# Performance work log

Measured on AMD Instinct MI355X. Metric: run time of the kernel, lower is better.

## Reference

```python
import jax, jax.numpy as jnp
import numpy as np

INF = 1.0e10
EPS = 1e-12

def setup_inputs() -> dict:
    key = jax.random.key(0)
    k1, k2 = jax.random.split(key)
    B, N, A = 512, 16384, 64
    return {
        "residue_ca_pos": jax.random.normal(k1, (B, N, 3), dtype=jnp.float32) * 10.0,
        "residue_mask": jnp.ones((B, N), dtype=jnp.float32),
        "atom_pos": jax.random.normal(k2, (B, A, 3), dtype=jnp.float32) * 10.0,
        "atom_mask": jnp.ones((B, A), dtype=jnp.float32),
        "max_p": 1,
        "top_k": 4096,
    }

def reference(residue_ca_pos, residue_mask, atom_pos, atom_mask, max_p, top_k):
    # ligand centroid per batch: [B, 3]
    centroid = atom_pos.sum(-2) / atom_mask.sum(-1, keepdims=True)
    # distance from centroid to each residue Ca, invalid residues pushed to +inf
    diff = centroid[:, None, :] - residue_ca_pos            # [B, N, 3]
    dists = jnp.sqrt(jnp.sum(diff * diff, axis=-1) + EPS) + (1.0 - residue_mask) * INF
    # k smallest distances -> neighbor indices [B, top_k]
    _, nbr_indices = jax.lax.top_k(-dists, top_k)
    rows = jnp.arange(residue_mask.shape[0])[:, None]       # [B, 1]
    # scatter writes building the masks (faithful to torch scatter_ with constants)
    residue_spatial_mask = residue_mask.at[rows, nbr_indices].set(0.0)
    residue_spatial_mask_esm = (1.0 - residue_mask).at[rows, nbr_indices].set(32.0)
    return residue_spatial_mask, residue_spatial_mask_esm
```

## Files before the change

### kernel.cpp

```cpp
#include <hip/hip_runtime.h>

#pragma clang fp contract(off)

#define B_  512
#define N_  16384
#define A_  64
#define SL  8
#define EPT 8
#define CAP 2048

__global__ __launch_bounds__(256) void k1_dist(
    const float* __restrict__ pos,  const float* __restrict__ mask,
    const float* __restrict__ apos, const float* __restrict__ amask,
    float* __restrict__ centws, unsigned* __restrict__ hist_g,
    unsigned short* __restrict__ ws16)
{
#pragma clang fp contract(off)
    __shared__ unsigned hist[2048];
    __shared__ float s_c[3];
    const int tid = threadIdx.x;
    const int blk = blockIdx.x;
    const int b = blk >> 3, sl = blk & 7;

#pragma unroll
    for (int i = 0; i < 8; ++i) hist[tid + i * 256] = 0u;

    if (tid < 64) {
        const float* ap = apos  + (size_t)b * (A_ * 3);
        const float* am = amask + (size_t)b * A_;
        float comp = 0.0f, ms = 0.0f;
        if (tid < 3) {
            comp = ap[tid];
            for (int a = 1; a < A_; ++a) comp += ap[a * 3 + tid];
        }
        if (tid == 3) {
            float r0 = am[0], r1 = am[1], r2 = am[2], r3 = am[3];
            float r4 = am[4], r5 = am[5], r6 = am[6], r7 = am[7];
            for (int i = 8; i < A_; i += 8) {
                r0 += am[i + 0]; r1 += am[i + 1]; r2 += am[i + 2]; r3 += am[i + 3];
                r4 += am[i + 4]; r5 += am[i + 5]; r6 += am[i + 6]; r7 += am[i + 7];
            }
            ms = ((r0 + r1) + (r2 + r3)) + ((r4 + r5) + (r6 + r7));
        }
        ms = __shfl(ms, 3, 64);
        if (tid < 3) s_c[tid] = comp / ms;
    }
    __syncthreads();
    if (sl == 0 && tid < 3) centws[b * 4 + tid] = s_c[tid];

    const float cx = s_c[0], cy = s_c[1], cz = s_c[2];
    const int base = b * N_ + sl * 2048 + tid * EPT;
    const float* __restrict__ p = pos  + (size_t)base * 3;
    const float* __restrict__ m = mask + base;

    unsigned bits[EPT];
#pragma unroll
    for (int g = 0; g < 2; ++g) {
        const float4 pa = *(const float4*)(p + g * 12);
        const float4 pb = *(const float4*)(p + g * 12 + 4);
        const float4 pc = *(const float4*)(p + g * 12 + 8);
        const float4 mv = *(const float4*)(m + g * 4);
        const float px[4] = {pa.x, pa.w, pb.z, pc.y};
        const float py[4] = {pa.y, pb.x, pb.w, pc.z};
        const float pz[4] = {pa.z, pb.y, pc.x, pc.w};
        const float mm[4] = {mv.x, mv.y, mv.z, mv.w};
#pragma unroll
        for (int j = 0; j < 4; ++j) {
            float dx = cx - px[j], dy = cy - py[j], dz = cz - pz[j];
            float dx2 = dx * dx, dy2 = dy * dy, dz2 = dz * dz;
            float s = (dx2 + dy2) + dz2;
            s = s + 1e-12f;
            float d = sqrtf(s);
            d = d + (1.0f - mm[j]) * 1e10f;
            bits[g * 4 + j] = __float_as_uint(d);
        }
    }
#pragma unroll
    for (int x = 0; x < EPT; ++x) atomicAdd(&hist[bits[x] >> 21], 1u);

    uint4 pk;
    pk.x = (bits[0] >> 16) | ((bits[1] >> 16) << 16);
    pk.y = (bits[2] >> 16) | ((bits[3] >> 16) << 16);
    pk.z = (bits[4] >> 16) | ((bits[5] >> 16) << 16);
    pk.w = (bits[6] >> 16) | ((bits[7] >> 16) << 16);
    *(uint4*)(ws16 + base) = pk;

    __syncthreads();
#pragma unroll
    for (int i = 0; i < 8; ++i) {
        const unsigned v = hist[tid + i * 256];
        if (v) atomicAdd(&hist_g[b * 2048 + tid + i * 256], v);
    }
}

__global__ __launch_bounds__(1024) void k2_select(
    const float* __restrict__ pos, const float* __restrict__ mask,
    const int* __restrict__ topk_ptr, const float* __restrict__ centws,
    const unsigned* __restrict__ hist_g, unsigned* __restrict__ P16arr,
    unsigned short* __restrict__ ws16)
{
#pragma clang fp contract(off)
    __shared__ unsigned       hist2[32];
    __shared__ unsigned       cand_bits[CAP];
    __shared__ unsigned short cand_idx[CAP];
    __shared__ float          s_c[3];
    __shared__ unsigned       s_B11, s_cum, s_P16, s_j, s_ncand, s_k;

    const int tid = threadIdx.x;
    const int b   = blockIdx.x;
    if (tid < 32) hist2[tid] = 0u;
    if (tid < 3)  s_c[tid] = centws[b * 4 + tid];
    if (tid == 0) {
        s_ncand = 0u;
        int kk = *topk_ptr;
        if (kk < 0)  kk = 0;
        if (kk > N_) kk = N_;
        s_k = (unsigned)kk;
    }
    __syncthreads();
    const unsigned k = s_k;
    if (k == 0u) { if (tid == 0) P16arr[b] = 0u; return; }

    if (tid < 64) {
        const uint4* hp = (const uint4*)(hist_g + (size_t)b * 2048 + tid * 32);
        unsigned ssum = 0;
#pragma unroll
        for (int r = 0; r < 8; ++r) { const uint4 h = hp[r]; ssum += h.x + h.y + h.z + h.w; }
        unsigned incl = ssum;
#pragma unroll
        for (int off = 1; off < 64; off <<= 1) {
            const unsigned v = (unsigned)__shfl_up((int)incl, off, 64);
            if (tid >= off) incl += v;
        }
        const unsigned long long bal = __ballot(incl >= k);
        const int g64 = __ffsll(bal) - 1;
        const unsigned cum64 = (unsigned)__shfl((int)(incl - ssum), g64, 64);
        const unsigned h2 = (tid < 32) ? hist_g[(size_t)b * 2048 + g64 * 32 + tid] : 0u;
        unsigned incl2 = h2;
#pragma unroll
        for (int off = 1; off < 64; off <<= 1) {
            const unsigned v = (unsigned)__shfl_up((int)incl2, off, 64);
            if (tid >= off) incl2 += v;
        }
        const unsigned long long bal2 = __ballot(tid < 32 && (cum64 + incl2 >= k));
        const int sb = __ffsll(bal2) - 1;
        const unsigned cum = cum64 + (unsigned)__shfl((int)(incl2 - h2), sb, 64);
        if (tid == 0) { s_B11 = (unsigned)(g64 * 32 + sb); s_cum = cum; }
    }
    __syncthreads();
    const unsigned B11 = s_B11;

    unsigned short* __restrict__ w16 = ws16 + (size_t)b * N_;
    const uint4* wp = (const uint4*)(w16 + (size_t)tid * 16);
    const uint4 a0 = wp[0];
    const uint4 a1 = wp[1];
    const unsigned pref[16] = {
        a0.x & 0xFFFFu, a0.x >> 16, a0.y & 0xFFFFu, a0.y >> 16,
        a0.z & 0xFFFFu, a0.z >> 16, a0.w & 0xFFFFu, a0.w >> 16,
        a1.x & 0xFFFFu, a1.x >> 16, a1.y & 0xFFFFu, a1.y >> 16,
        a1.z & 0xFFFFu, a1.z >> 16, a1.w & 0xFFFFu, a1.w >> 16 };
#pragma unroll
    for (int x = 0; x < 16; ++x)
        if ((pref[x] >> 5) == B11) atomicAdd(&hist2[pref[x] & 31u], 1u);
    __syncthreads();
    if (tid < 64) {
        const unsigned h = (tid < 32) ? hist2[tid] : 0u;
        unsigned incl = h;
#pragma unroll
        for (int off = 1; off < 64; off <<= 1) {
            const unsigned v = (unsigned)__shfl_up((int)incl, off, 64);
            if (tid >= off) incl += v;
        }
        const unsigned cum0 = s_cum;
        const unsigned long long bal = __ballot(tid < 32 && (cum0 + incl >= k));
        const int sb = __ffsll(bal) - 1;
        const unsigned cumx = cum0 + (unsigned)__shfl((int)(incl - h), sb, 64);
        if (tid == 0) { s_P16 = (B11 << 5) | (unsigned)sb; s_j = k - cumx; }
    }
    __syncthreads();
    const unsigned P16 = s_P16, j = s_j;

    const float cx = s_c[0], cy = s_c[1], cz = s_c[2];
    const float* __restrict__ p = pos  + (size_t)b * N_ * 3;
    const float* __restrict__ m = mask + (size_t)b * N_;
#pragma unroll
    for (int x = 0; x < 16; ++x) {
        if (pref[x] == P16) {
            const unsigned w = atomicAdd(&s_ncand, 1u);
            if (w < CAP) {
                const int i = tid * 16 + x;
                float dx = cx - p[i * 3], dy = cy - p[i * 3 + 1], dz = cz - p[i * 3 + 2];
                float dx2 = dx * dx, dy2 = dy * dy, dz2 = dz * dz;
                float s = (dx2 + dy2) + dz2;
                s = s + 1e-12f;
                float d = sqrtf(s);
                d = d + (1.0f - m[i]) * 1e10f;
                cand_bits[w] = __float_as_uint(d);
                cand_idx[w]  = (unsigned short)i;
            }
        }
    }
    __syncthreads();

    const unsigned c = min(s_ncand, (unsigned)CAP);
    for (unsigned t = tid; t < c; t += 1024) {
        const unsigned bt = cand_bits[t];
        const unsigned it = cand_idx[t];
        unsigned rank = 0;
        for (unsigned u = 0; u < c; ++u) {
            const unsigned bu = cand_bits[u];
            rank += (bu < bt) || (bu == bt && (unsigned)cand_idx[u] < it);
        }
        if (rank < j) w16[it] = 0;
    }
    if (tid == 0) P16arr[b] = P16;
}

__global__ __launch_bounds__(256) void k3_write(
    const float* __restrict__ mask, const unsigned* __restrict__ P16arr,
    const unsigned short* __restrict__ ws16,
    float* __restrict__ out0, float* __restrict__ out1)
{
    const int tid = threadIdx.x;
    const int blk = blockIdx.x;
    const int b = blk >> 3, sl = blk & 7;
    const int base = b * N_ + sl * 2048 + tid * EPT;
    const unsigned P16 = P16arr[b];

    const uint4  pk = *(const uint4*)(ws16 + base);
    const float4 m0 = *(const float4*)(mask + base);
    const float4 m1 = *(const float4*)(mask + base + 4);
    const unsigned pre[8] = {pk.x & 0xFFFFu, pk.x >> 16, pk.y & 0xFFFFu, pk.y >> 16,
                             pk.z & 0xFFFFu, pk.z >> 16, pk.w & 0xFFFFu, pk.w >> 16};
    const float mm[8] = {m0.x, m0.y, m0.z, m0.w, m1.x, m1.y, m1.z, m1.w};

    float o0v[8], o1v[8];
#pragma unroll
    for (int x = 0; x < 8; ++x) {
        const bool sel = pre[x] < P16;
        o0v[x] = sel ? 0.0f  : mm[x];
        o1v[x] = sel ? 32.0f : (1.0f - mm[x]);
    }
    *(float4*)(out0 + base)     = make_float4(o0v[0], o0v[1], o0v[2], o0v[3]);
    *(float4*)(out0 + base + 4) = make_float4(o0v[4], o0v[5], o0v[6], o0v[7]);
    *(float4*)(out1 + base)     = make_float4(o1v[0], o1v[1], o1v[2], o1v[3]);
    *(float4*)(out1 + base + 4) = make_float4(o1v[4], o1v[5], o1v[6], o1v[7]);
}

extern "C" void kernel_launch(void* const* d_in, const int* in_sizes, int n_in,
                              void* d_out, int out_size, void* d_ws, size_t ws_size,
                              hipStream_t stream) {
    const float* pos   = (const float*)d_in[0];
    const float* rmask = (const float*)d_in[1];
    const float* apos  = (const float*)d_in[2];
    const float* amask = (const float*)d_in[3];
    const int*   topk  = (const int*)d_in[5];

    float* out0 = (float*)d_out;
    float* out1 = out0 + (size_t)B_ * N_;

    char* ws = (char*)d_ws;
    float*          centws = (float*)ws;
    unsigned*       P16arr = (unsigned*)(ws + 8192);
    unsigned*       hist_g = (unsigned*)(ws + 16384);
    unsigned short* ws16   = (unsigned short*)(ws + 16384 + (size_t)B_ * 2048 * 4);

    hipMemsetAsync(hist_g, 0, (size_t)B_ * 2048 * sizeof(unsigned), stream);
    k1_dist  <<<B_ * SL, 256,  0, stream>>>(pos, rmask, apos, amask, centws, hist_g, ws16);
    k2_select<<<B_,      1024, 0, stream>>>(pos, rmask, topk, centws, hist_g, P16arr, ws16);
    k3_write <<<B_ * SL, 256,  0, stream>>>(rmask, P16arr, ws16, out0, out1);
}
```

Before: 235.4 us.

## Build coarse histogram in select kernel LDS; drop global histogram and memset

The 11-bit coarse histogram moves out of the distance kernel, where it was built with shared atomics and flushed to global memory with atomics after a memset. The select kernel now builds it in shared memory from the 16-bit prefixes it already loads. This removes the memset, the global atomic traffic and the extra histogram reads, at the cost of more shared-memory atomics per select block. The output kernel also switches to nontemporal vector stores so the streamed outputs do not pollute the cache.

```diff
diff --git a/kernel.cpp b/kernel.cpp
--- a/kernel.cpp
+++ b/kernel.cpp
@@ -9,21 +9,18 @@
 #define EPT 8
 #define CAP 2048
 
+typedef float  vfloat4 __attribute__((ext_vector_type(4)));
+
 __global__ __launch_bounds__(256) void k1_dist(
     const float* __restrict__ pos,  const float* __restrict__ mask,
     const float* __restrict__ apos, const float* __restrict__ amask,
-    float* __restrict__ centws, unsigned* __restrict__ hist_g,
-    unsigned short* __restrict__ ws16)
+    float* __restrict__ centws, unsigned short* __restrict__ ws16)
 {
 #pragma clang fp contract(off)
-    __shared__ unsigned hist[2048];
     __shared__ float s_c[3];
     const int tid = threadIdx.x;
     const int blk = blockIdx.x;
     const int b = blk >> 3, sl = blk & 7;
-
-#pragma unroll
-    for (int i = 0; i < 8; ++i) hist[tid + i * 256] = 0u;
 
     if (tid < 64) {
         const float* ap = apos  + (size_t)b * (A_ * 3);
@@ -75,31 +72,21 @@
             bits[g * 4 + j] = __float_as_uint(d);
         }
     }
-#pragma unroll
-    for (int x = 0; x < EPT; ++x) atomicAdd(&hist[bits[x] >> 21], 1u);
-
     uint4 pk;
     pk.x = (bits[0] >> 16) | ((bits[1] >> 16) << 16);
     pk.y = (bits[2] >> 16) | ((bits[3] >> 16) << 16);
     pk.z = (bits[4] >> 16) | ((bits[5] >> 16) << 16);
     pk.w = (bits[6] >> 16) | ((bits[7] >> 16) << 16);
     *(uint4*)(ws16 + base) = pk;
-
-    __syncthreads();
-#pragma unroll
-    for (int i = 0; i < 8; ++i) {
-        const unsigned v = hist[tid + i * 256];
-        if (v) atomicAdd(&hist_g[b * 2048 + tid + i * 256], v);
-    }
 }
 
 __global__ __launch_bounds__(1024) void k2_select(
     const float* __restrict__ pos, const float* __restrict__ mask,
     const int* __restrict__ topk_ptr, const float* __restrict__ centws,
-    const unsigned* __restrict__ hist_g, unsigned* __restrict__ P16arr,
-    unsigned short* __restrict__ ws16)
+    unsigned* __restrict__ P16arr, unsigned short* __restrict__ ws16)
 {
 #pragma clang fp contract(off)
+    __shared__ unsigned       hist[2048];
     __shared__ unsigned       hist2[32];
     __shared__ unsigned       cand_bits[CAP];
     __shared__ unsigned short cand_idx[CAP];
@@ -108,6 +95,7 @@
 
     const int tid = threadIdx.x;
     const int b   = blockIdx.x;
+    hist[tid] = 0u; hist[tid + 1024] = 0u;
     if (tid < 32) hist2[tid] = 0u;
     if (tid < 3)  s_c[tid] = centws[b * 4 + tid];
     if (tid == 0) {
@@ -120,35 +108,6 @@
     __syncthreads();
     const unsigned k = s_k;
     if (k == 0u) { if (tid == 0) P16arr[b] = 0u; return; }
-
-    if (tid < 64) {
-        const uint4* hp = (const uint4*)(hist_g + (size_t)b * 2048 + tid * 32);
-        unsigned ssum = 0;
-#pragma unroll
-        for (int r = 0; r < 8; ++r) { const uint4 h = hp[r]; ssum += h.x + h.y + h.z + h.w; }
-        unsigned incl = ssum;
-#pragma unroll
-        for (int off = 1; off < 64; off <<= 1) {
-            const unsigned v = (unsigned)__shfl_up((int)incl, off, 64);
-            if (tid >= off) incl += v;
-        }
-        const unsigned long long bal = __ballot(incl >= k);
-        const int g64 = __ffsll(bal) - 1;
-        const unsigned cum64 = (unsigned)__shfl((int)(incl - ssum), g64, 64);
-        const unsigned h2 = (tid < 32) ? hist_g[(size_t)b * 2048 + g64 * 32 + tid] : 0u;
-        unsigned incl2 = h2;
-#pragma unroll
-        for (int off = 1; off < 64; off <<= 1) {
-            const unsigned v = (unsigned)__shfl_up((int)incl2, off, 64);
-            if (tid >= off) incl2 += v;
-        }
-        const unsigned long long bal2 = __ballot(tid < 32 && (cum64 + incl2 >= k));
-        const int sb = __ffsll(bal2) - 1;
-        const unsigned cum = cum64 + (unsigned)__shfl((int)(incl2 - h2), sb, 64);
-        if (tid == 0) { s_B11 = (unsigned)(g64 * 32 + sb); s_cum = cum; }
-    }
-    __syncthreads();
-    const unsigned B11 = s_B11;
 
     unsigned short* __restrict__ w16 = ws16 + (size_t)b * N_;
     const uint4* wp = (const uint4*)(w16 + (size_t)tid * 16);
@@ -159,6 +118,39 @@
         a0.z & 0xFFFFu, a0.z >> 16, a0.w & 0xFFFFu, a0.w >> 16,
         a1.x & 0xFFFFu, a1.x >> 16, a1.y & 0xFFFFu, a1.y >> 16,
         a1.z & 0xFFFFu, a1.z >> 16, a1.w & 0xFFFFu, a1.w >> 16 };
+#pragma unroll
+    for (int x = 0; x < 16; ++x) atomicAdd(&hist[pref[x] >> 5], 1u);
+    __syncthreads();
+
+    if (tid < 64) {
+        const uint4* hp = (const uint4*)&hist[tid * 32];
+        unsigned ssum = 0;
+#pragma unroll
+        for (int r = 0; r < 8; ++r) { const uint4 h = hp[r]; ssum += h.x + h.y + h.z + h.w; }
+        unsigned incl = ssum;
+#pragma unroll
+        for (int off = 1; off < 64; off <<= 1) {
+            const unsigned v = (unsigned)__shfl_up((int)incl, off, 64);
+            if (tid >= off) incl += v;
+        }
+        const unsigned long long bal = __ballot(incl >= k);
+        const int g64 = __ffsll(bal) - 1;
+        const unsigned cum64 = (unsigned)__shfl((int)(incl - ssum), g64, 64);
+        const unsigned h2 = (tid < 32) ? hist[g64 * 32 + tid] : 0u;
+        unsigned incl2 = h2;
+#pragma unroll
+        for (int off = 1; off < 64; off <<= 1) {
+            const unsigned v = (unsigned)__shfl_up((int)incl2, off, 64);
+            if (tid >= off) incl2 += v;
+        }
+        const unsigned long long bal2 = __ballot(tid < 32 && (cum64 + incl2 >= k));
+        const int sb = __ffsll(bal2) - 1;
+        const unsigned cum = cum64 + (unsigned)__shfl((int)(incl2 - h2), sb, 64);
+        if (tid == 0) { s_B11 = (unsigned)(g64 * 32 + sb); s_cum = cum; }
+    }
+    __syncthreads();
+    const unsigned B11 = s_B11;
+
 #pragma unroll
     for (int x = 0; x < 16; ++x)
         if ((pref[x] >> 5) == B11) atomicAdd(&hist2[pref[x] & 31u], 1u);
@@ -234,17 +226,21 @@
                              pk.z & 0xFFFFu, pk.z >> 16, pk.w & 0xFFFFu, pk.w >> 16};
     const float mm[8] = {m0.x, m0.y, m0.z, m0.w, m1.x, m1.y, m1.z, m1.w};
 
-    float o0v[8], o1v[8];
+    float v0[8], v1[8];
 #pragma unroll
     for (int x = 0; x < 8; ++x) {
         const bool sel = pre[x] < P16;
-        o0v[x] = sel ? 0.0f  : mm[x];
-        o1v[x] = sel ? 32.0f : (1.0f - mm[x]);
-    }
-    *(float4*)(out0 + base)     = make_float4(o0v[0], o0v[1], o0v[2], o0v[3]);
-    *(float4*)(out0 + base + 4) = make_float4(o0v[4], o0v[5], o0v[6], o0v[7]);
-    *(float4*)(out1 + base)     = make_float4(o1v[0], o1v[1], o1v[2], o1v[3]);
-    *(float4*)(out1 + base + 4) = make_float4(o1v[4], o1v[5], o1v[6], o1v[7]);
+        v0[x] = sel ? 0.0f  : mm[x];
+        v1[x] = sel ? 32.0f : (1.0f - mm[x]);
+    }
+    const vfloat4 o0a = {v0[0], v0[1], v0[2], v0[3]};
+    const vfloat4 o0b = {v0[4], v0[5], v0[6], v0[7]};
+    const vfloat4 o1a = {v1[0], v1[1], v1[2], v1[3]};
+    const vfloat4 o1b = {v1[4], v1[5], v1[6], v1[7]};
+    __builtin_nontemporal_store(o0a, (vfloat4*)(out0 + base));
+    __builtin_nontemporal_store(o0b, (vfloat4*)(out0 + base + 4));
+    __builtin_nontemporal_store(o1a, (vfloat4*)(out1 + base));
+    __builtin_nontemporal_store(o1b, (vfloat4*)(out1 + base + 4));
 }
 
 extern "C" void kernel_launch(void* const* d_in, const int* in_sizes, int n_in,
@@ -262,11 +258,9 @@
     char* ws = (char*)d_ws;
     float*          centws = (float*)ws;
     unsigned*       P16arr = (unsigned*)(ws + 8192);
-    unsigned*       hist_g = (unsigned*)(ws + 16384);
-    unsigned short* ws16   = (unsigned short*)(ws + 16384 + (size_t)B_ * 2048 * 4);
-
-    hipMemsetAsync(hist_g, 0, (size_t)B_ * 2048 * sizeof(unsigned), stream);
-    k1_dist  <<<B_ * SL, 256,  0, stream>>>(pos, rmask, apos, amask, centws, hist_g, ws16);
-    k2_select<<<B_,      1024, 0, stream>>>(pos, rmask, topk, centws, hist_g, P16arr, ws16);
+    unsigned short* ws16   = (unsigned short*)(ws + 16384);
+
+    k1_dist  <<<B_ * SL, 256,  0, stream>>>(pos, rmask, apos, amask, centws, ws16);
+    k2_select<<<B_,      1024, 0, stream>>>(pos, rmask, topk, centws, P16arr, ws16);
     k3_write <<<B_ * SL, 256,  0, stream>>>(rmask, P16arr, ws16, out0, out1);
 }
```

Result: slower. 243.2 us (+3.3%).
